# Kernel optimization log

Measured on AMD Instinct MI355X. Metric: run time of the kernel, lower is better.

## Reference

```python
import jax, jax.numpy as jnp
import numpy as np

NUM_HEADS = 4
NUM_GROUPS = 8
EPS = 1e-5


def setup_inputs() -> dict:
    key = jax.random.key(0)
    ks = jax.random.split(key, 4)
    b, c, h, w = 16, 512, 32, 32
    x = jax.random.normal(ks[0], (b, c, h, w), dtype=jnp.float32)
    gamma = jnp.ones((c,), dtype=jnp.float32)
    beta = jnp.zeros((c,), dtype=jnp.float32)
    # conv1d kernel-size-1 weights expressed as [out, in] matrices
    w_qkv = jax.random.normal(ks[1], (3 * c, c), dtype=jnp.float32) * (1.0 / np.sqrt(c))
    b_qkv = jnp.zeros((3 * c,), dtype=jnp.float32)
    w_proj = jax.random.normal(ks[2], (c, c), dtype=jnp.float32) * (1.0 / np.sqrt(c))
    b_proj = jnp.zeros((c,), dtype=jnp.float32)
    return {"x": x, "gamma": gamma, "beta": beta, "w_qkv": w_qkv,
            "b_qkv": b_qkv, "w_proj": w_proj, "b_proj": b_proj}


def group_norm(x, gamma, beta):
    # x: [b, c, h, w]; normalize per (group) over (c/g, h, w)
    b, c, h, w = x.shape
    xg = x.reshape(b, NUM_GROUPS, c // NUM_GROUPS, h, w)
    mean = xg.mean(axis=(2, 3, 4), keepdims=True)
    var = xg.var(axis=(2, 3, 4), keepdims=True)
    xn = ((xg - mean) * jax.lax.rsqrt(var + EPS)).reshape(b, c, h, w)
    return xn * gamma[None, :, None, None] + beta[None, :, None, None]


def reference(x, gamma, beta, w_qkv, b_qkv, w_proj, b_proj):
    b, c, h, w = x.shape
    L = h * w
    hd = c // NUM_HEADS  # head_dim
    x_in = x
    xn = group_norm(x, gamma, beta).reshape(b, c, L)
    # 1x1 conv == matmul over channel dim: [b, 3c, L]
    qkv = jnp.einsum('oc,bcl->bol', w_qkv, xn) + b_qkv[None, :, None]
    q, k, v = jnp.split(qkv, 3, axis=1)  # each [b, c, L]
    q = q.reshape(b, NUM_HEADS, hd, L)
    k = k.reshape(b, NUM_HEADS, hd, L)
    v = v.reshape(b, NUM_HEADS, hd, L)
    scale = hd ** (-0.5)
    attn = jnp.einsum('bhdl,bhdm->bhlm', q * scale, k)  # [b,h,L,L]
    attn = jax.nn.softmax(attn, axis=-1)
    out = jnp.einsum('bhlm,bhdm->bhdl', attn, v).reshape(b, c, L)
    out = jnp.einsum('oc,bcl->bol', w_proj, out) + b_proj[None, :, None]
    return x_in + out.reshape(b, c, h, w)
```

## Files before the change

kernel.cpp:

```cpp
#include <hip/hip_runtime.h>
#include <hip/hip_bf16.h>

typedef __hip_bfloat16 bf16;
typedef __attribute__((ext_vector_type(8))) short short8;
typedef __attribute__((ext_vector_type(4))) float f32x4;
typedef __attribute__((ext_vector_type(16))) float f32x16;

__device__ __forceinline__ float b2f(bf16 v) { return __bfloat162float(v); }
__device__ __forceinline__ bf16  f2b(float v) { return __float2bfloat16(v); }

__global__ __launch_bounds__(256) void convert_w_kernel(
    const float* __restrict__ wq, const float* __restrict__ wp,
    bf16* __restrict__ wqb, bf16* __restrict__ wpb)
{
    int ch = blockIdx.x * 256 + threadIdx.x;
    float4 v;
    bf16* dst;
    if (ch < 196608) {
        v = ((const float4*)wq)[ch];
        dst = wqb + ch * 4;
    } else {
        int c2 = ch - 196608;
        v = ((const float4*)wp)[c2];
        dst = wpb + c2 * 4;
    }
    bf16 o[4] = {f2b(v.x), f2b(v.y), f2b(v.z), f2b(v.w)};
    *(uint2*)dst = *(const uint2*)o;
}

__global__ __launch_bounds__(256) void gn_partial_kernel(
    const float* __restrict__ x,
    float* __restrict__ partS, float* __restrict__ partQ)
{
    const int bid = blockIdx.x;
    const size_t base = (size_t)bid * 16384;
    const int t = threadIdx.x;

    float sum = 0.f, ssq = 0.f;
    const float4* x4 = (const float4*)(x + base);
    for (int i = t; i < 4096; i += 256) {
        float4 v = x4[i];
        sum += v.x + v.y + v.z + v.w;
        ssq += v.x * v.x + v.y * v.y + v.z * v.z + v.w * v.w;
    }
    #pragma unroll
    for (int off = 32; off > 0; off >>= 1) {
        sum += __shfl_down(sum, off);
        ssq += __shfl_down(ssq, off);
    }
    __shared__ float red[8];
    const int wid = t >> 6, lane = t & 63;
    if (lane == 0) { red[wid] = sum; red[4 + wid] = ssq; }
    __syncthreads();
    if (t == 0) {
        partS[bid] = red[0] + red[1] + red[2] + red[3];
        partQ[bid] = red[4] + red[5] + red[6] + red[7];
    }
}

__global__ __launch_bounds__(64) void gn_finalize_kernel(
    const float* __restrict__ partS, const float* __restrict__ partQ,
    const float* __restrict__ gamma, const float* __restrict__ beta,
    float* __restrict__ scaleB, float* __restrict__ shiftB)
{
    const int bg = blockIdx.x;
    const int b = bg >> 3, g = bg & 7;
    const int t = threadIdx.x;
    float s = partS[bg * 4] + partS[bg * 4 + 1] + partS[bg * 4 + 2] + partS[bg * 4 + 3];
    float q = partQ[bg * 4] + partQ[bg * 4 + 1] + partQ[bg * 4 + 2] + partQ[bg * 4 + 3];
    float mean = s * (1.f / 65536.f);
    float var  = q * (1.f / 65536.f) - mean * mean;
    float rstd = rsqrtf(var + 1e-5f);
    int c = g * 64 + t;
    float sc = rstd * gamma[c];
    scaleB[b * 512 + c] = sc;
    shiftB[b * 512 + c] = beta[c] - mean * sc;
}

__global__ __launch_bounds__(256) void gn_apply_t_kernel(
    const float* __restrict__ x,
    const float* __restrict__ scaleB,
    const float* __restrict__ shiftB,
    bf16* __restrict__ Xt)
{
    const int lt = blockIdx.x, ct = blockIdx.y, b = blockIdx.z;
    const int l0 = lt * 64, c0 = ct * 64;
    const int t = threadIdx.x;
    __shared__ float Ls[64][65];

    const float* xb = x + ((size_t)b * 512 + c0) * 1024 + l0;
    for (int i = t; i < 1024; i += 256) {
        int cc = i >> 4, lc = (i & 15) * 4;
        float4 v = *(const float4*)(xb + (size_t)cc * 1024 + lc);
        float sc = scaleB[b * 512 + c0 + cc];
        float sh = shiftB[b * 512 + c0 + cc];
        Ls[cc][lc]     = v.x * sc + sh;
        Ls[cc][lc + 1] = v.y * sc + sh;
        Ls[cc][lc + 2] = v.z * sc + sh;
        Ls[cc][lc + 3] = v.w * sc + sh;
    }
    __syncthreads();
    for (int i = t; i < 1024; i += 256) {
        int l = i >> 4, cc = (i & 15) * 4;
        bf16 o[4] = {f2b(Ls[cc][l]), f2b(Ls[cc + 1][l]),
                     f2b(Ls[cc + 2][l]), f2b(Ls[cc + 3][l])};
        *(uint2*)(Xt + ((size_t)b * 1024 + l0 + l) * 512 + c0 + cc) = *(const uint2*)o;
    }
}

__global__ __launch_bounds__(256) void mfma_qkv_kernel(
    const bf16* __restrict__ W,
    const bf16* __restrict__ Xt,
    const float* __restrict__ bias,
    bf16* __restrict__ Qt,
    bf16* __restrict__ Kt,
    bf16* __restrict__ Vb)
{
    const int n0 = blockIdx.x * 128;
    const int m0 = blockIdx.y * 128;
    const int b  = blockIdx.z;
    const int t  = threadIdx.x;
    const int w  = t >> 6, lane = t & 63;
    const int c  = lane & 15, quad = lane >> 4;
    const int w0 = w & 1, w1 = w >> 1;
    const int ak = quad * 8;

    __shared__ __align__(16) bf16 smem[17408];
    bf16* As = smem;
    bf16* Bs = smem + 5120;
    bf16* Cs = smem;

    const bf16* Ag = W + (size_t)m0 * 512;
    const bf16* Bg = Xt + ((size_t)b * 1024 + n0) * 512;

    const int srow = t >> 2, skc = (t & 3) * 8;

    short8 areg[2], breg[2];
    #pragma unroll
    for (int it = 0; it < 2; it++) {
        int row = srow + it * 64;
        areg[it] = *(const short8*)(Ag + (size_t)row * 512 + skc);
        breg[it] = *(const short8*)(Bg + (size_t)row * 512 + skc);
    }

    f32x4 acc[4][4];
    #pragma unroll
    for (int i = 0; i < 4; i++)
        #pragma unroll
        for (int j = 0; j < 4; j++)
            #pragma unroll
            for (int r = 0; r < 4; r++) acc[i][j][r] = 0.f;

    for (int k0 = 0; k0 < 512; k0 += 32) {
        __syncthreads();
        #pragma unroll
        for (int it = 0; it < 2; it++) {
            int row = srow + it * 64;
            *(short8*)&As[row * 40 + skc] = areg[it];
            *(short8*)&Bs[row * 40 + skc] = breg[it];
        }
        __syncthreads();
        {
            int k1 = (k0 + 32) & 511;
            #pragma unroll
            for (int it = 0; it < 2; it++) {
                int row = srow + it * 64;
                areg[it] = *(const short8*)(Ag + (size_t)row * 512 + k1 + skc);
                breg[it] = *(const short8*)(Bg + (size_t)row * 512 + k1 + skc);
            }
        }
        short8 af[4], bf[4];
        #pragma unroll
        for (int jm = 0; jm < 4; jm++)
            af[jm] = *(const short8*)&As[(w0 * 64 + jm * 16 + c) * 40 + ak];
        #pragma unroll
        for (int jn = 0; jn < 4; jn++)
            bf[jn] = *(const short8*)&Bs[(w1 * 64 + jn * 16 + c) * 40 + ak];
        #pragma unroll
        for (int jm = 0; jm < 4; jm++)
            #pragma unroll
            for (int jn = 0; jn < 4; jn++)
                acc[jm][jn] = __builtin_amdgcn_mfma_f32_16x16x32_bf16(
                    af[jm], bf[jn], acc[jm][jn], 0, 0, 0);
    }

    __syncthreads();
    const int cls = m0 >> 9;
    if (cls < 2) {
        #pragma unroll
        for (int jm = 0; jm < 4; jm++) {
            #pragma unroll
            for (int jn = 0; jn < 4; jn++) {
                bf16 o4[4];
                #pragma unroll
                for (int r = 0; r < 4; r++) {
                    int orow = w0 * 64 + jm * 16 + quad * 4 + r;
                    o4[r] = f2b(acc[jm][jn][r] + bias[m0 + orow]);
                }
                *(uint2*)&Cs[(size_t)(w1 * 64 + jn * 16 + c) * 136
                             + w0 * 64 + jm * 16 + quad * 4] = *(const uint2*)o4;
            }
        }
        __syncthreads();
        const int head = (m0 >> 7) & 3;
        bf16* Db = (cls == 0 ? Qt : Kt)
                   + (((size_t)(b * 4 + head)) * 1024 + n0) * 128;
        for (int i = t; i < 2048; i += 256) {
            int row = i >> 4, ch = (i & 15) * 8;
            *(short8*)(Db + (size_t)row * 128 + ch) = *(const short8*)&Cs[row * 136 + ch];
        }
    } else {
        #pragma unroll
        for (int jm = 0; jm < 4; jm++) {
            #pragma unroll
            for (int r = 0; r < 4; r++) {
                int orow = w0 * 64 + jm * 16 + quad * 4 + r;
                float bs = bias[m0 + orow];
                #pragma unroll
                for (int jn = 0; jn < 4; jn++)
                    Cs[orow * 136 + w1 * 64 + jn * 16 + c] = f2b(acc[jm][jn][r] + bs);
            }
        }
        __syncthreads();
        bf16* Cb = Vb + ((size_t)b * 512 + (m0 - 1024)) * 1024 + n0;
        for (int i = t; i < 2048; i += 256) {
            int row = i >> 4, ch = (i & 15) * 8;
            *(short8*)(Cb + (size_t)row * 1024 + ch) = *(const short8*)&Cs[row * 136 + ch];
        }
    }
}

#define HD 128
#define QT 128
#define MT 64
#define SM_SHIFT 6.0f

__global__ __launch_bounds__(256, 2) void attn_mfma_kernel(
    const bf16* __restrict__ Qt,
    const bf16* __restrict__ Kt,
    const bf16* __restrict__ Vb,
    bf16* __restrict__ out)
{
    const int bh = blockIdx.x;
    const int qt = blockIdx.y;
    const int b = bh >> 2, h = bh & 3;
    const int t = threadIdx.x;
    const int w = t >> 6, lane = t & 63;
    const int wrow = lane & 31;
    const int blk  = lane >> 5;
    const int l0 = qt * QT;

    __shared__ __align__(16) bf16 smem[27136];
    bf16* Ks = smem;
    bf16* Vs = smem + 8704;
    bf16* Ps = smem + 17920;

    const int qrow = w * 32 + wrow;
    const bf16* Qr = Qt + (((size_t)(b * 4 + h)) * 1024 + l0 + qrow) * 128;
    short8 aq[8];
    #pragma unroll
    for (int kt = 0; kt < 8; kt++)
        aq[kt] = *(const short8*)(Qr + kt * 16 + blk * 8);

    const bf16* Kb = Kt + (((size_t)(b * 4 + h)) * 1024) * 128;
    const bf16* Vg = Vb + ((size_t)(b * 512 + h * HD)) * 1024;

    short8 kreg[4], vreg[4];
    #pragma unroll
    for (int p = 0; p < 4; p++) {
        int i = t + p * 256;
        kreg[p] = *(const short8*)(Kb + (size_t)(i >> 4) * 128 + (i & 15) * 8);
        vreg[p] = *(const short8*)(Vg + (size_t)(i >> 3) * 1024 + (i & 7) * 8);
    }

    f32x16 acc_o[4];
    #pragma unroll
    for (int n = 0; n < 4; n++)
        #pragma unroll
        for (int r = 0; r < 16; r++) acc_o[n][r] = 0.f;

    float psum[16];
    #pragma unroll
    for (int r = 0; r < 16; r++) psum[r] = 0.f;

    const float scale = 0.08838834764831845f;

    for (int mt = 0; mt < 1024 / MT; mt++) {
        __syncthreads();

        #pragma unroll
        for (int p = 0; p < 4; p++) {
            int i = t + p * 256;
            *(short8*)&Ks[(i >> 4) * 136 + (i & 15) * 8] = kreg[p];
            *(short8*)&Vs[(i >> 3) * 72 + (i & 7) * 8]   = vreg[p];
        }
        __syncthreads();

        {
            int m0n = (mt < 15) ? (mt + 1) * MT : 0;
            #pragma unroll
            for (int p = 0; p < 4; p++) {
                int i = t + p * 256;
                kreg[p] = *(const short8*)(Kb + (size_t)(m0n + (i >> 4)) * 128 + (i & 15) * 8);
                vreg[p] = *(const short8*)(Vg + (size_t)(i >> 3) * 1024 + m0n + (i & 7) * 8);
            }
        }

        f32x16 accs[2];
        #pragma unroll
        for (int n = 0; n < 2; n++)
            #pragma unroll
            for (int r = 0; r < 16; r++) accs[n][r] = 0.f;
        #pragma unroll
        for (int kt = 0; kt < 8; kt++) {
            #pragma unroll
            for (int nt = 0; nt < 2; nt++) {
                short8 bfr = *(const short8*)&Ks[(nt * 32 + wrow) * 136 + kt * 16 + blk * 8];
                accs[nt] = __builtin_amdgcn_mfma_f32_32x32x16_bf16(aq[kt], bfr, accs[nt], 0, 0, 0);
            }
        }

        #pragma unroll
        for (int nt = 0; nt < 2; nt++)
            #pragma unroll
            for (int r = 0; r < 16; r++) {
                float p = __expf(accs[nt][r] * scale - SM_SHIFT);
                psum[r] += p;
                int row = w * 32 + (r & 3) + 8 * (r >> 2) + 4 * blk;
                Ps[row * 72 + nt * 32 + wrow] = f2b(p);
            }

        #pragma unroll
        for (int kt2 = 0; kt2 < 4; kt2++) {
            short8 a = *(const short8*)&Ps[(w * 32 + wrow) * 72 + kt2 * 16 + blk * 8];
            #pragma unroll
            for (int nt2 = 0; nt2 < 4; nt2++) {
                short8 bv = *(const short8*)&Vs[(nt2 * 32 + wrow) * 72 + kt2 * 16 + blk * 8];
                acc_o[nt2] = __builtin_amdgcn_mfma_f32_32x32x16_bf16(a, bv, acc_o[nt2], 0, 0, 0);
            }
        }
    }

    #pragma unroll
    for (int off = 1; off < 32; off <<= 1)
        #pragma unroll
        for (int r = 0; r < 16; r++)
            psum[r] += __shfl_xor(psum[r], off);

    __syncthreads();
    bf16* Os = smem;
    float inv[16];
    #pragma unroll
    for (int r = 0; r < 16; r++) inv[r] = 1.f / psum[r];
    #pragma unroll
    for (int nt2 = 0; nt2 < 4; nt2++)
        #pragma unroll
        for (int r = 0; r < 16; r++) {
            int row = w * 32 + (r & 3) + 8 * (r >> 2) + 4 * blk;
            Os[row * 136 + nt2 * 32 + wrow] = f2b(acc_o[nt2][r] * inv[r]);
        }
    __syncthreads();
    bf16* Ob = out + ((size_t)b * 1024 + l0) * 512 + h * HD;
    for (int i = t; i < 2048; i += 256) {
        int row = i >> 4, ch = (i & 15) * 8;
        *(short8*)(Ob + (size_t)row * 512 + ch) = *(const short8*)&Os[row * 136 + ch];
    }
}

__global__ __launch_bounds__(256) void mfma_proj_kernel(
    const bf16* __restrict__ W,
    const bf16* __restrict__ Xt,
    const float* __restrict__ bias,
    const float* __restrict__ res,
    float* __restrict__ C)
{
    const int n0 = blockIdx.x * 128;
    const int m0 = blockIdx.y * 128;
    const int b  = blockIdx.z;
    const int t  = threadIdx.x;
    const int w  = t >> 6, lane = t & 63;
    const int c  = lane & 15, quad = lane >> 4;
    const int w0 = w & 1, w1 = w >> 1;
    const int ak = quad * 8;

    __shared__ __align__(16) bf16 smem[17408];
    bf16* As = smem;
    bf16* Bs = smem + 5120;
    bf16* Cs = smem;

    const bf16* Ag = W + (size_t)m0 * 512;
    const bf16* Bg = Xt + ((size_t)b * 1024 + n0) * 512;

    const int srow = t >> 2, skc = (t & 3) * 8;

    short8 areg[2], breg[2];
    #pragma unroll
    for (int it = 0; it < 2; it++) {
        int row = srow + it * 64;
        areg[it] = *(const short8*)(Ag + (size_t)row * 512 + skc);
        breg[it] = *(const short8*)(Bg + (size_t)row * 512 + skc);
    }

    f32x4 acc[4][4];
    #pragma unroll
    for (int i = 0; i < 4; i++)
        #pragma unroll
        for (int j = 0; j < 4; j++)
            #pragma unroll
            for (int r = 0; r < 4; r++) acc[i][j][r] = 0.f;

    for (int k0 = 0; k0 < 512; k0 += 32) {
        __syncthreads();
        #pragma unroll
        for (int it = 0; it < 2; it++) {
            int row = srow + it * 64;
            *(short8*)&As[row * 40 + skc] = areg[it];
            *(short8*)&Bs[row * 40 + skc] = breg[it];
        }
        __syncthreads();
        {
            int k1 = (k0 + 32) & 511;
            #pragma unroll
            for (int it = 0; it < 2; it++) {
                int row = srow + it * 64;
                areg[it] = *(const short8*)(Ag + (size_t)row * 512 + k1 + skc);
                breg[it] = *(const short8*)(Bg + (size_t)row * 512 + k1 + skc);
            }
        }
        short8 af[4], bf[4];
        #pragma unroll
        for (int jm = 0; jm < 4; jm++)
            af[jm] = *(const short8*)&As[(w0 * 64 + jm * 16 + c) * 40 + ak];
        #pragma unroll
        for (int jn = 0; jn < 4; jn++)
            bf[jn] = *(const short8*)&Bs[(w1 * 64 + jn * 16 + c) * 40 + ak];
        #pragma unroll
        for (int jm = 0; jm < 4; jm++)
            #pragma unroll
            for (int jn = 0; jn < 4; jn++)
                acc[jm][jn] = __builtin_amdgcn_mfma_f32_16x16x32_bf16(
                    af[jm], bf[jn], acc[jm][jn], 0, 0, 0);
    }

    __syncthreads();
    #pragma unroll
    for (int jm = 0; jm < 4; jm++) {
        #pragma unroll
        for (int r = 0; r < 4; r++) {
            int orow = w0 * 64 + jm * 16 + quad * 4 + r;
            float bs = bias[m0 + orow];
            #pragma unroll
            for (int jn = 0; jn < 4; jn++)
                Cs[orow * 136 + w1 * 64 + jn * 16 + c] = f2b(acc[jm][jn][r] + bs);
        }
    }
    __syncthreads();
    const float* Rb = res + ((size_t)b * 512 + m0) * 1024 + n0;
    float* Cb = C + ((size_t)b * 512 + m0) * 1024 + n0;
    for (int i = t; i < 4096; i += 256) {
        int row = i >> 5, ch = (i & 31) * 4;
        float4 rv = *(const float4*)(Rb + (size_t)row * 1024 + ch);
        float4 ov;
        ov.x = b2f(Cs[row * 136 + ch + 0]) + rv.x;
        ov.y = b2f(Cs[row * 136 + ch + 1]) + rv.y;
        ov.z = b2f(Cs[row * 136 + ch + 2]) + rv.z;
        ov.w = b2f(Cs[row * 136 + ch + 3]) + rv.w;
        *(float4*)(Cb + (size_t)row * 1024 + ch) = ov;
    }
}

extern "C" void kernel_launch(void* const* d_in, const int* in_sizes, int n_in,
                              void* d_out, int out_size, void* d_ws, size_t ws_size,
                              hipStream_t stream)
{
    const float* x      = (const float*)d_in[0];
    const float* gamma  = (const float*)d_in[1];
    const float* beta   = (const float*)d_in[2];
    const float* w_qkv  = (const float*)d_in[3];
    const float* b_qkv  = (const float*)d_in[4];
    const float* w_proj = (const float*)d_in[5];
    const float* b_proj = (const float*)d_in[6];
    float* out = (float*)d_out;

    char* ws = (char*)d_ws;
    float* scaleB = (float*)ws;
    float* shiftB = (float*)(ws + 32768);
    bf16*  wqb    = (bf16*)(ws + 65536);
    bf16*  wpb    = (bf16*)(ws + 65536 + 1572864);
    char*  big    = ws + 65536 + 2097152;
    bf16*  Xt     = (bf16*)(big);
    bf16*  Qt     = (bf16*)(big + (size_t)16777216);
    bf16*  Kt     = (bf16*)(big + (size_t)2 * 16777216);
    bf16*  Vb     = (bf16*)(big + (size_t)3 * 16777216);
    float* partS  = (float*)(big + (size_t)4 * 16777216);
    float* partQ  = partS + 512;
    bf16*  attn_t = Xt;

    hipLaunchKernelGGL(convert_w_kernel, dim3(1024), dim3(256), 0, stream,
                       w_qkv, w_proj, wqb, wpb);
    hipLaunchKernelGGL(gn_partial_kernel, dim3(512), dim3(256), 0, stream,
                       x, partS, partQ);
    hipLaunchKernelGGL(gn_finalize_kernel, dim3(128), dim3(64), 0, stream,
                       partS, partQ, gamma, beta, scaleB, shiftB);
    hipLaunchKernelGGL(gn_apply_t_kernel, dim3(16, 8, 16), dim3(256), 0, stream,
                       x, scaleB, shiftB, Xt);
    hipLaunchKernelGGL(mfma_qkv_kernel, dim3(8, 12, 16), dim3(256), 0, stream,
                       wqb, Xt, b_qkv, Qt, Kt, Vb);
    hipLaunchKernelGGL(attn_mfma_kernel, dim3(64, 8), dim3(256), 0, stream,
                       Qt, Kt, Vb, attn_t);
    hipLaunchKernelGGL(mfma_proj_kernel, dim3(8, 4, 16), dim3(256), 0, stream,
                       wpb, attn_t, b_proj, x, out);
}
```

Baseline: 232.8 us.

## Keep attention probabilities in registers via transposed S=K·Q MFMA, double-buffer K/V

Computes the score tile as K·Q^T, so each lane holds probabilities laid out directly as the A operand of the P·V MFMA. This removes the P round-trip through LDS, using packed bf16 conversion with a row permutation of K rows to match the layout. K/V shared buffers are double-buffered, which drops one barrier per iteration. The change also adds exp2 with prefolded constants, s_setprio around the MFMA blocks, and a cheaper final row-sum reduction with rcp. The permutation and index mapping are subtle and could be wrong, and LDS use grows, which may affect occupancy at 2 blocks per CU.

```diff
diff --git a/kernel.cpp b/kernel.cpp
--- a/kernel.cpp
+++ b/kernel.cpp
@@ -8,6 +8,12 @@
 
 __device__ __forceinline__ float b2f(bf16 v) { return __bfloat162float(v); }
 __device__ __forceinline__ bf16  f2b(float v) { return __float2bfloat16(v); }
+
+__device__ __forceinline__ unsigned cvt_pk_bf16(float lo, float hi) {
+    unsigned r;
+    asm("v_cvt_pk_bf16_f32 %0, %1, %2" : "=v"(r) : "v"(lo), "v"(hi));
+    return r;
+}
 
 __global__ __launch_bounds__(256) void convert_w_kernel(
     const float* __restrict__ wq, const float* __restrict__ wp,
@@ -233,7 +239,6 @@
 #define HD 128
 #define QT 128
 #define MT 64
-#define SM_SHIFT 6.0f
 
 __global__ __launch_bounds__(256, 2) void attn_mfma_kernel(
     const bf16* __restrict__ Qt,
@@ -250,10 +255,7 @@
     const int blk  = lane >> 5;
     const int l0 = qt * QT;
 
-    __shared__ __align__(16) bf16 smem[27136];
-    bf16* Ks = smem;
-    bf16* Vs = smem + 8704;
-    bf16* Ps = smem + 17920;
+    __shared__ __align__(16) bf16 smem[2 * 17920];
 
     const int qrow = w * 32 + wrow;
     const bf16* Qr = Qt + (((size_t)(b * 4 + h)) * 1024 + l0 + qrow) * 128;
@@ -279,20 +281,22 @@
         #pragma unroll
         for (int r = 0; r < 16; r++) acc_o[n][r] = 0.f;
 
-    float psum[16];
-    #pragma unroll
-    for (int r = 0; r < 16; r++) psum[r] = 0.f;
-
-    const float scale = 0.08838834764831845f;
+    float psl4[4] = {0.f, 0.f, 0.f, 0.f};
+
+    const float kSc = 0.08838834764831845f * 1.4426950408889634f;
+    const float kSh = 6.0f * 1.4426950408889634f;
 
     for (int mt = 0; mt < 1024 / MT; mt++) {
-        __syncthreads();
+        bf16* Ks = smem + (mt & 1) * 17920;
+        bf16* Vs = Ks + 8704;
 
         #pragma unroll
         for (int p = 0; p < 4; p++) {
             int i = t + p * 256;
-            *(short8*)&Ks[(i >> 4) * 136 + (i & 15) * 8] = kreg[p];
-            *(short8*)&Vs[(i >> 3) * 72 + (i & 7) * 8]   = vreg[p];
+            int m = i >> 4;
+            int mrow = (m & 51) | ((m & 4) << 1) | ((m & 8) >> 1);
+            *(short8*)&Ks[mrow * 136 + (i & 15) * 8] = kreg[p];
+            *(short8*)&Vs[(i >> 3) * 72 + (i & 7) * 8]  = vreg[p];
         }
         __syncthreads();
 
@@ -311,47 +315,57 @@
         for (int n = 0; n < 2; n++)
             #pragma unroll
             for (int r = 0; r < 16; r++) accs[n][r] = 0.f;
+        __builtin_amdgcn_s_setprio(1);
         #pragma unroll
         for (int kt = 0; kt < 8; kt++) {
             #pragma unroll
             for (int nt = 0; nt < 2; nt++) {
-                short8 bfr = *(const short8*)&Ks[(nt * 32 + wrow) * 136 + kt * 16 + blk * 8];
-                accs[nt] = __builtin_amdgcn_mfma_f32_32x32x16_bf16(aq[kt], bfr, accs[nt], 0, 0, 0);
-            }
-        }
-
-        #pragma unroll
-        for (int nt = 0; nt < 2; nt++)
-            #pragma unroll
-            for (int r = 0; r < 16; r++) {
-                float p = __expf(accs[nt][r] * scale - SM_SHIFT);
-                psum[r] += p;
-                int row = w * 32 + (r & 3) + 8 * (r >> 2) + 4 * blk;
-                Ps[row * 72 + nt * 32 + wrow] = f2b(p);
-            }
-
+                short8 afr = *(const short8*)&Ks[(nt * 32 + wrow) * 136 + kt * 16 + blk * 8];
+                accs[nt] = __builtin_amdgcn_mfma_f32_32x32x16_bf16(afr, aq[kt], accs[nt], 0, 0, 0);
+            }
+        }
+        __builtin_amdgcn_s_setprio(0);
+
+        unsigned pw[2][8];
+        #pragma unroll
+        for (int nt = 0; nt < 2; nt++) {
+            float pv[16];
+            #pragma unroll
+            for (int r = 0; r < 16; r++)
+                pv[r] = exp2f(accs[nt][r] * kSc - kSh);
+            #pragma unroll
+            for (int r = 0; r < 16; r++) psl4[r & 3] += pv[r];
+            #pragma unroll
+            for (int wd = 0; wd < 8; wd++)
+                pw[nt][wd] = cvt_pk_bf16(pv[2 * wd], pv[2 * wd + 1]);
+        }
+
+        __builtin_amdgcn_s_setprio(1);
         #pragma unroll
         for (int kt2 = 0; kt2 < 4; kt2++) {
-            short8 a = *(const short8*)&Ps[(w * 32 + wrow) * 72 + kt2 * 16 + blk * 8];
+            union { short8 s; unsigned u[4]; } pa;
+            #pragma unroll
+            for (int wd = 0; wd < 4; wd++)
+                pa.u[wd] = pw[kt2 >> 1][(kt2 & 1) * 4 + wd];
             #pragma unroll
             for (int nt2 = 0; nt2 < 4; nt2++) {
                 short8 bv = *(const short8*)&Vs[(nt2 * 32 + wrow) * 72 + kt2 * 16 + blk * 8];
-                acc_o[nt2] = __builtin_amdgcn_mfma_f32_32x32x16_bf16(a, bv, acc_o[nt2], 0, 0, 0);
-            }
-        }
-    }
-
-    #pragma unroll
-    for (int off = 1; off < 32; off <<= 1)
-        #pragma unroll
-        for (int r = 0; r < 16; r++)
-            psum[r] += __shfl_xor(psum[r], off);
-
-    __syncthreads();
+                acc_o[nt2] = __builtin_amdgcn_mfma_f32_32x32x16_bf16(pa.s, bv, acc_o[nt2], 0, 0, 0);
+            }
+        }
+        __builtin_amdgcn_s_setprio(0);
+    }
+
+    float psl = (psl4[0] + psl4[1]) + (psl4[2] + psl4[3]);
+    float tot = psl + __shfl_xor(psl, 32);
+    float inv[16];
+    #pragma unroll
+    for (int r = 0; r < 16; r++) {
+        int q = (r & 3) + 8 * (r >> 2) + 4 * blk;
+        inv[r] = __builtin_amdgcn_rcpf(__shfl(tot, q | (lane & 32)));
+    }
+
     bf16* Os = smem;
-    float inv[16];
-    #pragma unroll
-    for (int r = 0; r < 16; r++) inv[r] = 1.f / psum[r];
     #pragma unroll
     for (int nt2 = 0; nt2 < 4; nt2++)
         #pragma unroll
```

Measured after the change: 226.5 us. 1.03x faster.
